# Kernel optimization log

Measured on AMD Instinct MI355X. Metric: run time of the kernel, lower is better.

Reference implementation:

```python
import jax, jax.numpy as jnp
import numpy as np

N = 50000   # nodes
E = 800000  # edges
G = 64      # graphs
D_IN = 128
D_OUT = 64
HID = 2 * D_OUT  # 128, hidden width of non-final layers
EPS = 1e-5


def _seg_sum(v, idx, n):
    return jax.ops.segment_sum(v, idx, num_segments=n)


def _gcn(x, W, b, src, dst, n):
    # GCNConv with default add_self_loops=True, edge_weight=1, sym norm
    xw = x @ W                                            # [N, out]
    deg = _seg_sum(jnp.ones(src.shape[0], x.dtype), dst, n) + 1.0  # +1 self loop
    dis = jax.lax.rsqrt(deg)                              # deg^{-1/2}, deg>=1
    norm = dis[src] * dis[dst]                            # [E]
    agg = _seg_sum(norm[:, None] * xw[src], dst, n)       # gather-scale-scatter
    return agg + (dis * dis)[:, None] * xw + b            # self-loop term + bias


def _mpnn_layer(x, src, dst, edge_attr, gw, gb, ew, eb, n):
    h = _gcn(x, gw, gb, src, dst, n)
    e = jax.nn.relu(edge_attr[:, None] * ew + eb)         # Linear(1,out).relu per edge
    msg = h[src] + e                                      # message = x_j + edge_attr
    cnt = _seg_sum(jnp.ones(src.shape[0], x.dtype), dst, n)
    return _seg_sum(msg, dst, n) / jnp.clip(cnt, 1.0)[:, None]  # scatter-mean


def _ln(x, g, b):
    # node-wise LayerNorm over feature dim
    mu = x.mean(-1, keepdims=True)
    var = x.var(-1, keepdims=True)
    return (x - mu) * jax.lax.rsqrt(var + EPS) * g + b


def setup_inputs() -> dict:
    key = jax.random.key(0)
    ks = jax.random.split(key, 24)
    x = jax.random.normal(ks[0], (N, D_IN), jnp.float32)
    edge_index = jax.random.randint(ks[1], (2, E), 0, N, dtype=jnp.int64)
    edge_attr = jax.random.uniform(ks[2], (E,), jnp.float32)
    batch = jnp.sort(jax.random.randint(ks[3], (N,), 0, G, dtype=jnp.int64))

    def lin(k, fan_in, shape):
        return jax.random.uniform(k, shape, jnp.float32, -1.0, 1.0) / np.sqrt(fan_in)

    # layer 0: in 128 -> 128; layer 1: 128 -> 128; layer 2: 128 -> 64
    inp = {
        "x": x, "edge_index": edge_index, "edge_attr": edge_attr, "batch": batch,
        "gcn_w0": lin(ks[4], D_IN, (D_IN, HID)),  "gcn_b0": jnp.zeros((HID,), jnp.float32),
        "edge_w0": lin(ks[5], 1, (HID,)),          "edge_b0": lin(ks[6], 1, (HID,)),
        "ln_g0": jnp.ones((HID,), jnp.float32),   "ln_b0": jnp.zeros((HID,), jnp.float32),
        "gcn_w1": lin(ks[7], HID, (HID, HID)),    "gcn_b1": jnp.zeros((HID,), jnp.float32),
        "edge_w1": lin(ks[8], 1, (HID,)),          "edge_b1": lin(ks[9], 1, (HID,)),
        "ln_g1": jnp.ones((HID,), jnp.float32),   "ln_b1": jnp.zeros((HID,), jnp.float32),
        "gcn_w2": lin(ks[10], HID, (HID, D_OUT)), "gcn_b2": jnp.zeros((D_OUT,), jnp.float32),
        "edge_w2": lin(ks[11], 1, (D_OUT,)),       "edge_b2": lin(ks[12], 1, (D_OUT,)),
    }
    return inp


def reference(x, edge_index, edge_attr, batch,
              gcn_w0, gcn_b0, edge_w0, edge_b0, ln_g0, ln_b0,
              gcn_w1, gcn_b1, edge_w1, edge_b1, ln_g1, ln_b1,
              gcn_w2, gcn_b2, edge_w2, edge_b2):
    src, dst = edge_index[0], edge_index[1]
    h = _mpnn_layer(x, src, dst, edge_attr, gcn_w0, gcn_b0, edge_w0, edge_b0, N)
    h = _ln(jax.nn.relu(h), ln_g0, ln_b0)
    h = _mpnn_layer(h, src, dst, edge_attr, gcn_w1, gcn_b1, edge_w1, edge_b1, N)
    h = _ln(jax.nn.relu(h), ln_g1, ln_b1)
    h = _mpnn_layer(h, src, dst, edge_attr, gcn_w2, gcn_b2, edge_w2, edge_b2, N)
    # global_mean_pool
    cnt = _seg_sum(jnp.ones((N,), h.dtype), batch, G)
    z_pooled = _seg_sum(h, batch, G) / jnp.clip(cnt, 1.0)[:, None]
    return h, z_pooled
```

## Files before the change

### kernel.cpp

```cpp
#include <hip/hip_runtime.h>

#define NN 50000
#define NE 800000
#define NG 64
#define HID 128
#define DOUT 64
#define LN_EPS 1e-5f
#define NBUK 391
#define BCAP 3072
#define EPB 2048

typedef unsigned int uint32;
typedef unsigned short ushort16;
typedef __attribute__((ext_vector_type(8))) short bf16x8;
typedef __attribute__((ext_vector_type(4))) float f32x4;

__device__ inline ushort16 f2bf(float f) {
  uint32 u = __float_as_uint(f);
  u += 0x7fffu + ((u >> 16) & 1u);
  return (ushort16)(u >> 16);
}
__device__ inline uint32 pack2(float x, float y) {
  return (uint32)f2bf(x) | ((uint32)f2bf(y) << 16);
}
__device__ inline float bflo(uint32 p) { return __uint_as_float(p << 16); }
__device__ inline float bfhi(uint32 p) { return __uint_as_float(p & 0xffff0000u); }

__global__ __launch_bounds__(256) void k_init(float* __restrict__ Z, int* __restrict__ bcur) {
  int i = blockIdx.x * 256 + threadIdx.x;
  if (i < NG * 64) Z[i] = 0.f;
  if (i < NBUK) bcur[i] = i * BCAP;
}

__global__ __launch_bounds__(1024) void k_bucket(const int* __restrict__ src,
                                                 const int* __restrict__ dst,
                                                 const float* __restrict__ ea,
                                                 int* __restrict__ bcur,
                                                 uint2* __restrict__ tmp, int e) {
  __shared__ int hist[NBUK], lbase[NBUK], lcur[NBUK];
  int t = threadIdx.x;
  for (int i = t; i < NBUK; i += 1024) {
    hist[i] = 0;
    lcur[i] = 0;
  }
  __syncthreads();
  int base_e = blockIdx.x * EPB;
  int dstv[EPB / 1024];
#pragma unroll
  for (int k = 0; k < EPB / 1024; k++) {
    int i = base_e + k * 1024 + t;
    int d = (i < e) ? dst[i] : -1;
    dstv[k] = d;
    if (d >= 0) atomicAdd(&hist[d >> 7], 1);
  }
  __syncthreads();
  for (int i = t; i < NBUK; i += 1024) {
    int c = hist[i];
    int b = 0;
    if (c > 0) b = atomicAdd(&bcur[i], c);
    lbase[i] = b;
  }
  __syncthreads();
#pragma unroll
  for (int k = 0; k < EPB / 1024; k++) {
    int i = base_e + k * 1024 + t;
    int d = dstv[k];
    if (d >= 0) {
      int b = d >> 7;
      int r = atomicAdd(&lcur[b], 1);
      int pos = lbase[b] + r;
      if (pos < (b + 1) * BCAP) {
        uint2 rec;
        rec.x = (uint32)(src[i] & 0xffff) | ((uint32)(d & 127) << 16);
        rec.y = __float_as_uint(ea[i]);
        tmp[pos] = rec;
      }
    }
  }
}

__global__ __launch_bounds__(512) void k_bscan(const int* __restrict__ bcur,
                                               int* __restrict__ bbase,
                                               int* __restrict__ rowptr) {
  __shared__ int s[512];
  int t = threadIdx.x;
  int v = 0;
  if (t < NBUK) {
    v = bcur[t] - t * BCAP;
    if (v > BCAP) v = BCAP;
  }
  s[t] = v;
  __syncthreads();
  for (int off = 1; off < 512; off <<= 1) {
    int x = (t >= off) ? s[t - off] : 0;
    __syncthreads();
    s[t] += x;
    __syncthreads();
  }
  if (t < NBUK) bbase[t] = s[t] - v;
  if (t == 511) {
    bbase[NBUK] = s[511];
    rowptr[NN] = s[511];
  }
}

__global__ __launch_bounds__(256) void k_bsort(const uint2* __restrict__ tmp,
                                               const int* __restrict__ bcur,
                                               const int* __restrict__ bbase,
                                               int* __restrict__ rowptr,
                                               int* __restrict__ csrc,
                                               uint2* __restrict__ emsg,
                                               float* __restrict__ dis,
                                               float* __restrict__ invc) {
  int b = blockIdx.x;
  __shared__ int hist[128], excl[128], cur[128];
  int t = threadIdx.x;
  if (t < 128) {
    hist[t] = 0;
    cur[t] = 0;
  }
  __syncthreads();
  int cnt = bcur[b] - b * BCAP;
  if (cnt > BCAP) cnt = BCAP;
  int tb = b * BCAP;
  int ob = bbase[b];
  for (int i = t; i < cnt; i += 256) {
    uint2 r = tmp[tb + i];
    atomicAdd(&hist[(r.x >> 16) & 127], 1);
  }
  __syncthreads();
  int myDeg = (t < 128) ? hist[t] : 0;
  for (int off = 1; off < 128; off <<= 1) {
    int x = 0;
    if (t < 128 && t >= off) x = hist[t - off];
    __syncthreads();
    if (t < 128) hist[t] += x;
    __syncthreads();
  }
  if (t < 128) {
    excl[t] = hist[t] - myDeg;
    int node = (b << 7) + t;
    if (node < NN) {
      rowptr[node] = ob + excl[t];
      dis[node] = rsqrtf((float)(myDeg + 1));
      invc[node] = (myDeg > 0) ? 1.0f / (float)myDeg : 1.0f;
    }
  }
  __syncthreads();
  for (int i = t; i < cnt; i += 256) {
    uint2 r = tmp[tb + i];
    int o = (r.x >> 16) & 127;
    int p = atomicAdd(&cur[o], 1);
    int pos = ob + excl[o] + p;
    int s = (int)(r.x & 0xffffu);
    csrc[pos] = s;
    emsg[pos] = make_uint2((uint32)s, r.y);
  }
}

template <int FOUT, bool IN_BF, bool OUT_BF>
__global__ __launch_bounds__(256) void k_gemm(const void* __restrict__ Xv,
                                              const float* __restrict__ W,
                                              const float* __restrict__ dis,
                                              void* __restrict__ Yv, int n) {
  const int NT = FOUT / 16;
  __shared__ __align__(16) unsigned short Wt[FOUT][136];
  __shared__ __align__(16) unsigned short Xs[64][136];
  int t = threadIdx.x;
  int row0 = blockIdx.x * 64;
  for (int idx = t; idx < 128 * FOUT; idx += 256) {
    int k = idx / FOUT, col = idx % FOUT;
    Wt[col][k] = (unsigned short)f2bf(W[idx]);
  }
  if (IN_BF) {
    const uint32* Xb = (const uint32*)Xv;
    for (int idx = t; idx < 64 * 64; idx += 256) {
      int r = idx >> 6, c = idx & 63;
      uint32 v = (row0 + r < n) ? Xb[(size_t)(row0 + r) * 64 + c] : 0u;
      *(uint32*)&Xs[r][c * 2] = v;
    }
  } else {
    const float* Xf = (const float*)Xv;
    for (int idx = t; idx < 64 * 64; idx += 256) {
      int r = idx >> 6, c = idx & 63;
      float2 v = make_float2(0.f, 0.f);
      if (row0 + r < n) v = ((const float2*)(Xf + (size_t)(row0 + r) * 128))[c];
      *(uint32*)&Xs[r][c * 2] = pack2(v.x, v.y);
    }
  }
  __syncthreads();
  int lane = t & 63, wv = t >> 6;
  int mrow = lane & 15, q = lane >> 4;
  f32x4 acc[NT];
#pragma unroll
  for (int c = 0; c < NT; c++) acc[c] = (f32x4){0.f, 0.f, 0.f, 0.f};
#pragma unroll
  for (int kt = 0; kt < 4; kt++) {
    bf16x8 af = *(const bf16x8*)&Xs[wv * 16 + mrow][kt * 32 + q * 8];
#pragma unroll
    for (int c = 0; c < NT; c++) {
      bf16x8 bfg = *(const bf16x8*)&Wt[c * 16 + mrow][kt * 32 + q * 8];
      acc[c] = __builtin_amdgcn_mfma_f32_16x16x32_bf16(af, bfg, acc[c], 0, 0, 0);
    }
  }
  float ds[4];
#pragma unroll
  for (int r = 0; r < 4; r++) {
    int rg = row0 + wv * 16 + q * 4 + r;
    ds[r] = (rg < n) ? dis[rg] : 0.f;
  }
#pragma unroll
  for (int c = 0; c < NT; c++) {
    int cg = c * 16 + mrow;
#pragma unroll
    for (int r = 0; r < 4; r++) {
      int rg = row0 + wv * 16 + q * 4 + r;
      if (rg < n) {
        float v = acc[c][r] * ds[r];
        if (OUT_BF)
          ((unsigned short*)Yv)[(size_t)rg * FOUT + cg] = (unsigned short)f2bf(v);
        else
          ((float*)Yv)[(size_t)rg * FOUT + cg] = v;
      }
    }
  }
}

__global__ __launch_bounds__(256) void k_agg_bf(const uint2* __restrict__ XW2,
                                                const float* __restrict__ dis,
                                                const int* __restrict__ rowptr,
                                                const int* __restrict__ csrc,
                                                const float* __restrict__ bias,
                                                uint2* __restrict__ Hb2, int n) {
  int l = threadIdx.x & 31;
  int node = blockIdx.x * 8 + (threadIdx.x >> 5);
  if (node >= n) return;
  float dn = dis[node];
  int beg = rowptr[node], end = rowptr[node + 1];
  float a0 = 0.f, a1 = 0.f, a2 = 0.f, a3 = 0.f;
  int i = beg;
  for (; i + 8 <= end; i += 8) {
    int s[8];
    uint2 p[8];
#pragma unroll
    for (int k = 0; k < 8; k++) s[k] = csrc[i + k];
#pragma unroll
    for (int k = 0; k < 8; k++) p[k] = XW2[(size_t)s[k] * 32 + l];
#pragma unroll
    for (int k = 0; k < 8; k++) {
      a0 += bflo(p[k].x);
      a1 += bfhi(p[k].x);
      a2 += bflo(p[k].y);
      a3 += bfhi(p[k].y);
    }
  }
  for (; i < end; i++) {
    uint2 p = XW2[(size_t)csrc[i] * 32 + l];
    a0 += bflo(p.x);
    a1 += bfhi(p.x);
    a2 += bflo(p.y);
    a3 += bfhi(p.y);
  }
  uint2 ps = XW2[(size_t)node * 32 + l];
  float4 bb = ((const float4*)bias)[l];
  float h0 = dn * (a0 + bflo(ps.x)) + bb.x;
  float h1 = dn * (a1 + bfhi(ps.x)) + bb.y;
  float h2 = dn * (a2 + bflo(ps.y)) + bb.z;
  float h3 = dn * (a3 + bfhi(ps.y)) + bb.w;
  Hb2[(size_t)node * 32 + l] = make_uint2(pack2(h0, h1), pack2(h2, h3));
}

__global__ __launch_bounds__(256) void k_msg_bf(const uint2* __restrict__ Hb2,
                                                const float* __restrict__ ew,
                                                const float* __restrict__ eb,
                                                const int* __restrict__ rowptr,
                                                const uint2* __restrict__ emsg,
                                                const float* __restrict__ invc,
                                                const float* __restrict__ lng,
                                                const float* __restrict__ lnb,
                                                uint2* __restrict__ OUTb2, int n) {
  int l = threadIdx.x & 31;
  int node = blockIdx.x * 8 + (threadIdx.x >> 5);
  if (node >= n) return;
  int beg = rowptr[node], end = rowptr[node + 1];
  float4 w = ((const float4*)ew)[l];
  float4 b = ((const float4*)eb)[l];
  float a0 = 0.f, a1 = 0.f, a2 = 0.f, a3 = 0.f;
  int i = beg;
  for (; i + 8 <= end; i += 8) {
    uint2 m[8];
    uint2 p[8];
#pragma unroll
    for (int k = 0; k < 8; k++) m[k] = emsg[i + k];
#pragma unroll
    for (int k = 0; k < 8; k++) p[k] = Hb2[(size_t)m[k].x * 32 + l];
#pragma unroll
    for (int k = 0; k < 8; k++) {
      float a = __uint_as_float(m[k].y);
      a0 += bflo(p[k].x) + fmaxf(a * w.x + b.x, 0.f);
      a1 += bfhi(p[k].x) + fmaxf(a * w.y + b.y, 0.f);
      a2 += bflo(p[k].y) + fmaxf(a * w.z + b.z, 0.f);
      a3 += bfhi(p[k].y) + fmaxf(a * w.w + b.w, 0.f);
    }
  }
  for (; i < end; i++) {
    uint2 m = emsg[i];
    uint2 p = Hb2[(size_t)m.x * 32 + l];
    float a = __uint_as_float(m.y);
    a0 += bflo(p.x) + fmaxf(a * w.x + b.x, 0.f);
    a1 += bfhi(p.x) + fmaxf(a * w.y + b.y, 0.f);
    a2 += bflo(p.y) + fmaxf(a * w.z + b.z, 0.f);
    a3 += bfhi(p.y) + fmaxf(a * w.w + b.w, 0.f);
  }
  float ic = invc[node];
  float o0 = fmaxf(a0 * ic, 0.f), o1 = fmaxf(a1 * ic, 0.f);
  float o2 = fmaxf(a2 * ic, 0.f), o3 = fmaxf(a3 * ic, 0.f);
  float s1 = o0 + o1 + o2 + o3;
  float s2 = o0 * o0 + o1 * o1 + o2 * o2 + o3 * o3;
#pragma unroll
  for (int off = 16; off; off >>= 1) {
    s1 += __shfl_xor(s1, off, 64);
    s2 += __shfl_xor(s2, off, 64);
  }
  float mu = s1 * (1.f / 128.f);
  float var = s2 * (1.f / 128.f) - mu * mu;
  float r = rsqrtf(var + LN_EPS);
  float4 g = ((const float4*)lng)[l];
  float4 bb = ((const float4*)lnb)[l];
  o0 = (o0 - mu) * r * g.x + bb.x;
  o1 = (o1 - mu) * r * g.y + bb.y;
  o2 = (o2 - mu) * r * g.z + bb.z;
  o3 = (o3 - mu) * r * g.w + bb.w;
  OUTb2[(size_t)node * 32 + l] = make_uint2(pack2(o0, o1), pack2(o2, o3));
}

__global__ __launch_bounds__(256) void k_agg64b(const uint32* __restrict__ XWb,
                                                const float* __restrict__ dis,
                                                const int* __restrict__ rowptr,
                                                const int* __restrict__ csrc,
                                                const float* __restrict__ bias,
                                                uint32* __restrict__ Hb, int n) {
  int l = threadIdx.x & 31;
  int node = blockIdx.x * 8 + (threadIdx.x >> 5);
  if (node >= n) return;
  float dn = dis[node];
  int beg = rowptr[node], end = rowptr[node + 1];
  float a0 = 0.f, a1 = 0.f;
  int i = beg;
  for (; i + 8 <= end; i += 8) {
    int s[8];
    uint32 p[8];
#pragma unroll
    for (int k = 0; k < 8; k++) s[k] = csrc[i + k];
#pragma unroll
    for (int k = 0; k < 8; k++) p[k] = XWb[(size_t)s[k] * 32 + l];
#pragma unroll
    for (int k = 0; k < 8; k++) {
      a0 += bflo(p[k]);
      a1 += bfhi(p[k]);
    }
  }
  for (; i < end; i++) {
    uint32 p = XWb[(size_t)csrc[i] * 32 + l];
    a0 += bflo(p);
    a1 += bfhi(p);
  }
  uint32 ps = XWb[(size_t)node * 32 + l];
  float2 bb = ((const float2*)bias)[l];
  float h0 = dn * (a0 + bflo(ps)) + bb.x;
  float h1 = dn * (a1 + bfhi(ps)) + bb.y;
  Hb[(size_t)node * 32 + l] = pack2(h0, h1);
}

__global__ __launch_bounds__(256) void k_msg64b(const uint32* __restrict__ Hb,
                                                const float* __restrict__ ew,
                                                const float* __restrict__ eb,
                                                const int* __restrict__ rowptr,
                                                const uint2* __restrict__ emsg,
                                                const float* __restrict__ invc,
                                                float* __restrict__ OUT, int n) {
  int l = threadIdx.x & 31;
  int node = blockIdx.x * 8 + (threadIdx.x >> 5);
  if (node >= n) return;
  int beg = rowptr[node], end = rowptr[node + 1];
  float2 w = ((const float2*)ew)[l];
  float2 b = ((const float2*)eb)[l];
  float a0 = 0.f, a1 = 0.f;
  int i = beg;
  for (; i + 8 <= end; i += 8) {
    uint2 m[8];
    uint32 p[8];
#pragma unroll
    for (int k = 0; k < 8; k++) m[k] = emsg[i + k];
#pragma unroll
    for (int k = 0; k < 8; k++) p[k] = Hb[(size_t)m[k].x * 32 + l];
#pragma unroll
    for (int k = 0; k < 8; k++) {
      float a = __uint_as_float(m[k].y);
      a0 += bflo(p[k]) + fmaxf(a * w.x + b.x, 0.f);
      a1 += bfhi(p[k]) + fmaxf(a * w.y + b.y, 0.f);
    }
  }
  for (; i < end; i++) {
    uint2 m = emsg[i];
    uint32 p = Hb[(size_t)m.x * 32 + l];
    float a = __uint_as_float(m.y);
    a0 += bflo(p) + fmaxf(a * w.x + b.x, 0.f);
    a1 += bfhi(p) + fmaxf(a * w.y + b.y, 0.f);
  }
  float ic = invc[node];
  ((float2*)OUT)[(size_t)node * 32 + l] = make_float2(a0 * ic, a1 * ic);
}

#define POOL_BLOCKS 256
__global__ __launch_bounds__(256) void k_pool_partial(const float* __restrict__ H,
                                                      const int* __restrict__ batch,
                                                      float* __restrict__ Z, int n) {
  int lane = threadIdx.x & 63;
  int wid = blockIdx.x * 4 + (threadIdx.x >> 6);
  const int WAVES = POOL_BLOCKS * 4;
  int per = (n + WAVES - 1) / WAVES;
  int beg = wid * per;
  int end = beg + per;
  if (end > n) end = n;
  if (beg >= end) return;
  int g = batch[beg];
  float acc = 0.f;
  for (int i = beg; i < end; i++) {
    int gi = batch[i];
    if (gi != g) {
      atomicAdd(&Z[g * 64 + lane], acc);
      acc = 0.f;
      g = gi;
    }
    acc += H[(size_t)i * 64 + lane];
  }
  atomicAdd(&Z[g * 64 + lane], acc);
}

__global__ __launch_bounds__(64) void k_pool_div(float* __restrict__ Z,
                                                 const int* __restrict__ batch, int n) {
  int g = blockIdx.x;
  __shared__ int scnt;
  if (threadIdx.x == 0) {
    int lo = 0, hi = n;
    while (lo < hi) { int m = (lo + hi) >> 1; if (batch[m] < g) lo = m + 1; else hi = m; }
    int b0 = lo;
    lo = 0; hi = n;
    while (lo < hi) { int m = (lo + hi) >> 1; if (batch[m] < g + 1) lo = m + 1; else hi = m; }
    scnt = lo - b0;
  }
  __syncthreads();
  float c = (float)scnt;
  if (c < 1.f) c = 1.f;
  Z[g * 64 + threadIdx.x] /= c;
}

extern "C" void kernel_launch(void* const* d_in, const int* in_sizes, int n_in,
                              void* d_out, int out_size, void* d_ws, size_t ws_size,
                              hipStream_t stream) {
  const float* x = (const float*)d_in[0];
  const int* ei = (const int*)d_in[1];
  const float* ea = (const float*)d_in[2];
  const int* batch = (const int*)d_in[3];
  const float* gw0 = (const float*)d_in[4];
  const float* gb0 = (const float*)d_in[5];
  const float* ew0 = (const float*)d_in[6];
  const float* eb0 = (const float*)d_in[7];
  const float* lg0 = (const float*)d_in[8];
  const float* lb0 = (const float*)d_in[9];
  const float* gw1 = (const float*)d_in[10];
  const float* gb1 = (const float*)d_in[11];
  const float* ew1 = (const float*)d_in[12];
  const float* eb1 = (const float*)d_in[13];
  const float* lg1 = (const float*)d_in[14];
  const float* lb1 = (const float*)d_in[15];
  const float* gw2 = (const float*)d_in[16];
  const float* gb2 = (const float*)d_in[17];
  const float* ew2 = (const float*)d_in[18];
  const float* eb2 = (const float*)d_in[19];
  float* out = (float*)d_out;

  const int* src = ei;
  const int* dst = ei + NE;

  char* w = (char*)d_ws;
  size_t off = 0;
  auto alloc = [&](size_t bytes) -> void* {
    void* p = (void*)(w + off);
    off = (off + bytes + 255) & ~(size_t)255;
    return p;
  };
  int* rowptr = (int*)alloc((NN + 1) * sizeof(int));
  int* bcur = (int*)alloc(NBUK * sizeof(int));
  int* bbase = (int*)alloc((NBUK + 1) * sizeof(int));
  int* csrc = (int*)alloc(NE * sizeof(int));
  uint2* emsg = (uint2*)alloc(NE * sizeof(uint2));
  float* dis = (float*)alloc(NN * sizeof(float));
  float* invc = (float*)alloc(NN * sizeof(float));
  uint2* B1b = (uint2*)alloc((size_t)NN * 32 * sizeof(uint2));
  uint2* B2b = (uint2*)alloc((size_t)NN * 32 * sizeof(uint2));
  uint32* F1b = (uint32*)alloc((size_t)NN * 32 * sizeof(uint32));
  uint32* F2b = (uint32*)alloc((size_t)NN * 32 * sizeof(uint32));
  uint2* tmp = (uint2*)alloc((size_t)NBUK * BCAP * sizeof(uint2));

  float* Z = out + (size_t)NN * 64;

  hipLaunchKernelGGL(k_init, dim3((NG * 64 + 255) / 256), dim3(256), 0, stream, Z, bcur);
  hipLaunchKernelGGL(k_bucket, dim3((NE + EPB - 1) / EPB), dim3(1024), 0, stream, src, dst, ea,
                     bcur, tmp, NE);
  hipLaunchKernelGGL(k_bscan, dim3(1), dim3(512), 0, stream, bcur, bbase, rowptr);
  hipLaunchKernelGGL(k_bsort, dim3(NBUK), dim3(256), 0, stream, tmp, bcur, bbase, rowptr, csrc,
                     emsg, dis, invc);

  dim3 gemm_grid((NN + 63) / 64), tb(256);
  dim3 node_grid((NN + 7) / 8);

  hipLaunchKernelGGL((k_gemm<128, false, true>), gemm_grid, tb, 0, stream, x, gw0, dis, B1b, NN);
  hipLaunchKernelGGL(k_agg_bf, node_grid, tb, 0, stream, B1b, dis, rowptr, csrc, gb0, B2b, NN);
  hipLaunchKernelGGL(k_msg_bf, node_grid, tb, 0, stream, B2b, ew0, eb0, rowptr, emsg, invc,
                     lg0, lb0, B1b, NN);
  hipLaunchKernelGGL((k_gemm<128, true, true>), gemm_grid, tb, 0, stream, B1b, gw1, dis, B2b, NN);
  hipLaunchKernelGGL(k_agg_bf, node_grid, tb, 0, stream, B2b, dis, rowptr, csrc, gb1, B1b, NN);
  hipLaunchKernelGGL(k_msg_bf, node_grid, tb, 0, stream, B1b, ew1, eb1, rowptr, emsg, invc,
                     lg1, lb1, B2b, NN);
  hipLaunchKernelGGL((k_gemm<64, true, true>), gemm_grid, tb, 0, stream, B2b, gw2, dis, F1b, NN);
  hipLaunchKernelGGL(k_agg64b, node_grid, tb, 0, stream, F1b, dis, rowptr, csrc, gb2, F2b, NN);
  hipLaunchKernelGGL(k_msg64b, node_grid, tb, 0, stream, F2b, ew2, eb2, rowptr, emsg, invc,
                     out, NN);
  hipLaunchKernelGGL(k_pool_partial, dim3(POOL_BLOCKS), tb, 0, stream, out, batch, Z, NN);
  hipLaunchKernelGGL(k_pool_div, dim3(NG), dim3(64), 0, stream, Z, batch, NN);
}
```

Measured before the change: 427.1 us.

## Split gather kernels into feature-column slices and defer LayerNorm into next GEMM

The aggregation and message kernels now process each node in two feature halves, with consecutive blocks (slice = blockIdx.x & 1) covering the two halves of the same nodes. Each block's gathers therefore touch a narrower column band of the feature table, which is meant to improve cache locality and give more parallel blocks. Because LayerNorm needs full-row statistics, the message kernel now writes partial sums, a new small kernel combines them into mean and inverse std, and the normalisation is applied while loading inputs in the following GEMM. The cost is extra launches, duplicated index and edge-record reads across slices, and extra traffic for the statistics buffers.

Result: slower. 487.7 us (+14.2%).

```diff
diff --git a/kernel.cpp b/kernel.cpp
--- a/kernel.cpp
+++ b/kernel.cpp
@@ -158,11 +158,14 @@
   }
 }
 
-template <int FOUT, bool IN_BF, bool OUT_BF>
+template <int FOUT, bool IN_BF, bool LN_IN>
 __global__ __launch_bounds__(256) void k_gemm(const void* __restrict__ Xv,
                                               const float* __restrict__ W,
                                               const float* __restrict__ dis,
-                                              void* __restrict__ Yv, int n) {
+                                              const float2* __restrict__ musd,
+                                              const float* __restrict__ lng,
+                                              const float* __restrict__ lnb,
+                                              unsigned short* __restrict__ Yv, int n) {
   const int NT = FOUT / 16;
   __shared__ __align__(16) unsigned short Wt[FOUT][136];
   __shared__ __align__(16) unsigned short Xs[64][136];
@@ -176,8 +179,22 @@
     const uint32* Xb = (const uint32*)Xv;
     for (int idx = t; idx < 64 * 64; idx += 256) {
       int r = idx >> 6, c = idx & 63;
-      uint32 v = (row0 + r < n) ? Xb[(size_t)(row0 + r) * 64 + c] : 0u;
-      *(uint32*)&Xs[r][c * 2] = v;
+      int rg = row0 + r;
+      uint32 v = 0u;
+      float2 ms = make_float2(0.f, 0.f);
+      if (rg < n) {
+        v = Xb[(size_t)rg * 64 + c];
+        if (LN_IN) ms = musd[rg];
+      }
+      if (LN_IN) {
+        float2 g = ((const float2*)lng)[c];
+        float2 q = ((const float2*)lnb)[c];
+        float lo = (bflo(v) - ms.x) * ms.y * g.x + q.x;
+        float hi = (bfhi(v) - ms.x) * ms.y * g.y + q.y;
+        *(uint32*)&Xs[r][c * 2] = pack2(lo, hi);
+      } else {
+        *(uint32*)&Xs[r][c * 2] = v;
+      }
     }
   } else {
     const float* Xf = (const float*)Xv;
@@ -215,134 +232,22 @@
 #pragma unroll
     for (int r = 0; r < 4; r++) {
       int rg = row0 + wv * 16 + q * 4 + r;
-      if (rg < n) {
-        float v = acc[c][r] * ds[r];
-        if (OUT_BF)
-          ((unsigned short*)Yv)[(size_t)rg * FOUT + cg] = (unsigned short)f2bf(v);
-        else
-          ((float*)Yv)[(size_t)rg * FOUT + cg] = v;
-      }
-    }
-  }
-}
-
-__global__ __launch_bounds__(256) void k_agg_bf(const uint2* __restrict__ XW2,
+      if (rg < n) Yv[(size_t)rg * FOUT + cg] = (unsigned short)f2bf(acc[c][r] * ds[r]);
+    }
+  }
+}
+
+__global__ __launch_bounds__(256) void k_agg_bf(const uint32* __restrict__ XW,
                                                 const float* __restrict__ dis,
                                                 const int* __restrict__ rowptr,
                                                 const int* __restrict__ csrc,
                                                 const float* __restrict__ bias,
-                                                uint2* __restrict__ Hb2, int n) {
+                                                uint32* __restrict__ H, int n) {
+  int slice = blockIdx.x & 1;
   int l = threadIdx.x & 31;
-  int node = blockIdx.x * 8 + (threadIdx.x >> 5);
+  int node = (blockIdx.x >> 1) * 8 + (threadIdx.x >> 5);
   if (node >= n) return;
-  float dn = dis[node];
-  int beg = rowptr[node], end = rowptr[node + 1];
-  float a0 = 0.f, a1 = 0.f, a2 = 0.f, a3 = 0.f;
-  int i = beg;
-  for (; i + 8 <= end; i += 8) {
-    int s[8];
-    uint2 p[8];
-#pragma unroll
-    for (int k = 0; k < 8; k++) s[k] = csrc[i + k];
-#pragma unroll
-    for (int k = 0; k < 8; k++) p[k] = XW2[(size_t)s[k] * 32 + l];
-#pragma unroll
-    for (int k = 0; k < 8; k++) {
-      a0 += bflo(p[k].x);
-      a1 += bfhi(p[k].x);
-      a2 += bflo(p[k].y);
-      a3 += bfhi(p[k].y);
-    }
-  }
-  for (; i < end; i++) {
-    uint2 p = XW2[(size_t)csrc[i] * 32 + l];
-    a0 += bflo(p.x);
-    a1 += bfhi(p.x);
-    a2 += bflo(p.y);
-    a3 += bfhi(p.y);
-  }
-  uint2 ps = XW2[(size_t)node * 32 + l];
-  float4 bb = ((const float4*)bias)[l];
-  float h0 = dn * (a0 + bflo(ps.x)) + bb.x;
-  float h1 = dn * (a1 + bfhi(ps.x)) + bb.y;
-  float h2 = dn * (a2 + bflo(ps.y)) + bb.z;
-  float h3 = dn * (a3 + bfhi(ps.y)) + bb.w;
-  Hb2[(size_t)node * 32 + l] = make_uint2(pack2(h0, h1), pack2(h2, h3));
-}
-
-__global__ __launch_bounds__(256) void k_msg_bf(const uint2* __restrict__ Hb2,
-                                                const float* __restrict__ ew,
-                                                const float* __restrict__ eb,
-                                                const int* __restrict__ rowptr,
-                                                const uint2* __restrict__ emsg,
-                                                const float* __restrict__ invc,
-                                                const float* __restrict__ lng,
-                                                const float* __restrict__ lnb,
-                                                uint2* __restrict__ OUTb2, int n) {
-  int l = threadIdx.x & 31;
-  int node = blockIdx.x * 8 + (threadIdx.x >> 5);
-  if (node >= n) return;
-  int beg = rowptr[node], end = rowptr[node + 1];
-  float4 w = ((const float4*)ew)[l];
-  float4 b = ((const float4*)eb)[l];
-  float a0 = 0.f, a1 = 0.f, a2 = 0.f, a3 = 0.f;
-  int i = beg;
-  for (; i + 8 <= end; i += 8) {
-    uint2 m[8];
-    uint2 p[8];
-#pragma unroll
-    for (int k = 0; k < 8; k++) m[k] = emsg[i + k];
-#pragma unroll
-    for (int k = 0; k < 8; k++) p[k] = Hb2[(size_t)m[k].x * 32 + l];
-#pragma unroll
-    for (int k = 0; k < 8; k++) {
-      float a = __uint_as_float(m[k].y);
-      a0 += bflo(p[k].x) + fmaxf(a * w.x + b.x, 0.f);
-      a1 += bfhi(p[k].x) + fmaxf(a * w.y + b.y, 0.f);
-      a2 += bflo(p[k].y) + fmaxf(a * w.z + b.z, 0.f);
-      a3 += bfhi(p[k].y) + fmaxf(a * w.w + b.w, 0.f);
-    }
-  }
-  for (; i < end; i++) {
-    uint2 m = emsg[i];
-    uint2 p = Hb2[(size_t)m.x * 32 + l];
-    float a = __uint_as_float(m.y);
-    a0 += bflo(p.x) + fmaxf(a * w.x + b.x, 0.f);
-    a1 += bfhi(p.x) + fmaxf(a * w.y + b.y, 0.f);
-    a2 += bflo(p.y) + fmaxf(a * w.z + b.z, 0.f);
-    a3 += bfhi(p.y) + fmaxf(a * w.w + b.w, 0.f);
-  }
-  float ic = invc[node];
-  float o0 = fmaxf(a0 * ic, 0.f), o1 = fmaxf(a1 * ic, 0.f);
-  float o2 = fmaxf(a2 * ic, 0.f), o3 = fmaxf(a3 * ic, 0.f);
-  float s1 = o0 + o1 + o2 + o3;
-  float s2 = o0 * o0 + o1 * o1 + o2 * o2 + o3 * o3;
-#pragma unroll
-  for (int off = 16; off; off >>= 1) {
-    s1 += __shfl_xor(s1, off, 64);
-    s2 += __shfl_xor(s2, off, 64);
-  }
-  float mu = s1 * (1.f / 128.f);
-  float var = s2 * (1.f / 128.f) - mu * mu;
-  float r = rsqrtf(var + LN_EPS);
-  float4 g = ((const float4*)lng)[l];
-  float4 bb = ((const float4*)lnb)[l];
-  o0 = (o0 - mu) * r * g.x + bb.x;
-  o1 = (o1 - mu) * r * g.y + bb.y;
-  o2 = (o2 - mu) * r * g.z + bb.z;
-  o3 = (o3 - mu) * r * g.w + bb.w;
-  OUTb2[(size_t)node * 32 + l] = make_uint2(pack2(o0, o1), pack2(o2, o3));
-}
-
-__global__ __launch_bounds__(256) void k_agg64b(const uint32* __restrict__ XWb,
-                                                const float* __restrict__ dis,
-                                                const int* __restrict__ rowptr,
-                                                const int* __restrict__ csrc,
-                                                const float* __restrict__ bias,
-                                                uint32* __restrict__ Hb, int n) {
-  int l = threadIdx.x & 31;
-  int node = blockIdx.x * 8 + (threadIdx.x >> 5);
-  if (node >= n) return;
+  const uint32* T = XW + slice * 32 + l;
   float dn = dis[node];
   int beg = rowptr[node], end = rowptr[node + 1];
   float a0 = 0.f, a1 = 0.f;
@@ -353,7 +258,7 @@
 #pragma unroll
     for (int k = 0; k < 8; k++) s[k] = csrc[i + k];
 #pragma unroll
-    for (int k = 0; k < 8; k++) p[k] = XWb[(size_t)s[k] * 32 + l];
+    for (int k = 0; k < 8; k++) p[k] = T[(size_t)s[k] * 64];
 #pragma unroll
     for (int k = 0; k < 8; k++) {
       a0 += bflo(p[k]);
@@ -361,15 +266,119 @@
     }
   }
   for (; i < end; i++) {
-    uint32 p = XWb[(size_t)csrc[i] * 32 + l];
+    uint32 p = T[(size_t)csrc[i] * 64];
     a0 += bflo(p);
     a1 += bfhi(p);
   }
-  uint32 ps = XWb[(size_t)node * 32 + l];
-  float2 bb = ((const float2*)bias)[l];
+  uint32 ps = T[(size_t)node * 64];
+  float2 bb = ((const float2*)bias)[slice * 32 + l];
   float h0 = dn * (a0 + bflo(ps)) + bb.x;
   float h1 = dn * (a1 + bfhi(ps)) + bb.y;
-  Hb[(size_t)node * 32 + l] = pack2(h0, h1);
+  H[(size_t)node * 64 + slice * 32 + l] = pack2(h0, h1);
+}
+
+__global__ __launch_bounds__(256) void k_msg_bf(const uint32* __restrict__ Hb,
+                                                const float* __restrict__ ew,
+                                                const float* __restrict__ eb,
+                                                const int* __restrict__ rowptr,
+                                                const uint2* __restrict__ emsg,
+                                                const float* __restrict__ invc,
+                                                uint32* __restrict__ OUT,
+                                                float2* __restrict__ s1s2, int n) {
+  int slice = blockIdx.x & 1;
+  int l = threadIdx.x & 31;
+  int node = (blockIdx.x >> 1) * 8 + (threadIdx.x >> 5);
+  if (node >= n) return;
+  const uint32* T = Hb + slice * 32 + l;
+  int beg = rowptr[node], end = rowptr[node + 1];
+  float2 w = ((const float2*)ew)[slice * 32 + l];
+  float2 b = ((const float2*)eb)[slice * 32 + l];
+  float a0 = 0.f, a1 = 0.f;
+  int i = beg;
+  for (; i + 8 <= end; i += 8) {
+    uint2 m[8];
+    uint32 p[8];
+#pragma unroll
+    for (int k = 0; k < 8; k++) m[k] = emsg[i + k];
+#pragma unroll
+    for (int k = 0; k < 8; k++) p[k] = T[(size_t)m[k].x * 64];
+#pragma unroll
+    for (int k = 0; k < 8; k++) {
+      float e = __uint_as_float(m[k].y);
+      a0 += bflo(p[k]) + fmaxf(e * w.x + b.x, 0.f);
+      a1 += bfhi(p[k]) + fmaxf(e * w.y + b.y, 0.f);
+    }
+  }
+  for (; i < end; i++) {
+    uint2 m = emsg[i];
+    uint32 p = T[(size_t)m.x * 64];
+    float e = __uint_as_float(m.y);
+    a0 += bflo(p) + fmaxf(e * w.x + b.x, 0.f);
+    a1 += bfhi(p) + fmaxf(e * w.y + b.y, 0.f);
+  }
+  float ic = invc[node];
+  float o0 = fmaxf(a0 * ic, 0.f);
+  float o1 = fmaxf(a1 * ic, 0.f);
+  OUT[(size_t)node * 64 + slice * 32 + l] = pack2(o0, o1);
+  float s1 = o0 + o1, s2 = o0 * o0 + o1 * o1;
+#pragma unroll
+  for (int off = 16; off; off >>= 1) {
+    s1 += __shfl_xor(s1, off, 64);
+    s2 += __shfl_xor(s2, off, 64);
+  }
+  if (l == 0) s1s2[(size_t)node * 2 + slice] = make_float2(s1, s2);
+}
+
+__global__ __launch_bounds__(256) void k_lnstat(const float2* __restrict__ s1s2,
+                                                float2* __restrict__ musd, int n) {
+  int i = blockIdx.x * 256 + threadIdx.x;
+  if (i < n) {
+    float2 a = s1s2[(size_t)i * 2];
+    float2 b = s1s2[(size_t)i * 2 + 1];
+    float mu = (a.x + b.x) * (1.f / 128.f);
+    float var = (a.y + b.y) * (1.f / 128.f) - mu * mu;
+    musd[i] = make_float2(mu, rsqrtf(var + LN_EPS));
+  }
+}
+
+__global__ __launch_bounds__(256) void k_agg64b(const uint32* __restrict__ XW,
+                                                const float* __restrict__ dis,
+                                                const int* __restrict__ rowptr,
+                                                const int* __restrict__ csrc,
+                                                const float* __restrict__ bias,
+                                                uint32* __restrict__ H, int n) {
+  int slice = blockIdx.x & 1;
+  int l = threadIdx.x & 15;
+  int node = (blockIdx.x >> 1) * 16 + (threadIdx.x >> 4);
+  if (node >= n) return;
+  const uint32* T = XW + slice * 16 + l;
+  float dn = dis[node];
+  int beg = rowptr[node], end = rowptr[node + 1];
+  float a0 = 0.f, a1 = 0.f;
+  int i = beg;
+  for (; i + 8 <= end; i += 8) {
+    int s[8];
+    uint32 p[8];
+#pragma unroll
+    for (int k = 0; k < 8; k++) s[k] = csrc[i + k];
+#pragma unroll
+    for (int k = 0; k < 8; k++) p[k] = T[(size_t)s[k] * 32];
+#pragma unroll
+    for (int k = 0; k < 8; k++) {
+      a0 += bflo(p[k]);
+      a1 += bfhi(p[k]);
+    }
+  }
+  for (; i < end; i++) {
+    uint32 p = T[(size_t)csrc[i] * 32];
+    a0 += bflo(p);
+    a1 += bfhi(p);
+  }
+  uint32 ps = T[(size_t)node * 32];
+  float2 bb = ((const float2*)bias)[slice * 16 + l];
+  float h0 = dn * (a0 + bflo(ps)) + bb.x;
+  float h1 = dn * (a1 + bfhi(ps)) + bb.y;
+  H[(size_t)node * 32 + slice * 16 + l] = pack2(h0, h1);
 }
 
 __global__ __launch_bounds__(256) void k_msg64b(const uint32* __restrict__ Hb,
@@ -379,12 +388,14 @@
                                                 const uint2* __restrict__ emsg,
                                                 const float* __restrict__ invc,
                                                 float* __restrict__ OUT, int n) {
-  int l = threadIdx.x & 31;
-  int node = blockIdx.x * 8 + (threadIdx.x >> 5);
+  int slice = blockIdx.x & 1;
+  int l = threadIdx.x & 15;
+  int node = (blockIdx.x >> 1) * 16 + (threadIdx.x >> 4);
   if (node >= n) return;
+  const uint32* T = Hb + slice * 16 + l;
   int beg = rowptr[node], end = rowptr[node + 1];
-  float2 w = ((const float2*)ew)[l];
-  float2 b = ((const float2*)eb)[l];
+  float2 w = ((const float2*)ew)[slice * 16 + l];
+  float2 b = ((const float2*)eb)[slice * 16 + l];
   float a0 = 0.f, a1 = 0.f;
   int i = beg;
   for (; i + 8 <= end; i += 8) {
@@ -393,23 +404,23 @@
 #pragma unroll
     for (int k = 0; k < 8; k++) m[k] = emsg[i + k];
 #pragma unroll
-    for (int k = 0; k < 8; k++) p[k] = Hb[(size_t)m[k].x * 32 + l];
+    for (int k = 0; k < 8; k++) p[k] = T[(size_t)m[k].x * 32];
 #pragma unroll
     for (int k = 0; k < 8; k++) {
-      float a = __uint_as_float(m[k].y);
-      a0 += bflo(p[k]) + fmaxf(a * w.x + b.x, 0.f);
-      a1 += bfhi(p[k]) + fmaxf(a * w.y + b.y, 0.f);
+      float e = __uint_as_float(m[k].y);
+      a0 += bflo(p[k]) + fmaxf(e * w.x + b.x, 0.f);
+      a1 += bfhi(p[k]) + fmaxf(e * w.y + b.y, 0.f);
     }
   }
   for (; i < end; i++) {
     uint2 m = emsg[i];
-    uint32 p = Hb[(size_t)m.x * 32 + l];
-    float a = __uint_as_float(m.y);
-    a0 += bflo(p) + fmaxf(a * w.x + b.x, 0.f);
-    a1 += bfhi(p) + fmaxf(a * w.y + b.y, 0.f);
+    uint32 p = T[(size_t)m.x * 32];
+    float e = __uint_as_float(m.y);
+    a0 += bflo(p) + fmaxf(e * w.x + b.x, 0.f);
+    a1 += bfhi(p) + fmaxf(e * w.y + b.y, 0.f);
   }
   float ic = invc[node];
-  ((float2*)OUT)[(size_t)node * 32 + l] = make_float2(a0 * ic, a1 * ic);
+  ((float2*)OUT)[(size_t)node * 32 + slice * 16 + l] = make_float2(a0 * ic, a1 * ic);
 }
 
 #define POOL_BLOCKS 256
@@ -498,8 +509,10 @@
   uint2* emsg = (uint2*)alloc(NE * sizeof(uint2));
   float* dis = (float*)alloc(NN * sizeof(float));
   float* invc = (float*)alloc(NN * sizeof(float));
-  uint2* B1b = (uint2*)alloc((size_t)NN * 32 * sizeof(uint2));
-  uint2* B2b = (uint2*)alloc((size_t)NN * 32 * sizeof(uint2));
+  float2* s1s2 = (float2*)alloc((size_t)NN * 2 * sizeof(float2));
+  float2* musd = (float2*)alloc((size_t)NN * sizeof(float2));
+  uint32* B1b = (uint32*)alloc((size_t)NN * 64 * sizeof(uint32));
+  uint32* B2b = (uint32*)alloc((size_t)NN * 64 * sizeof(uint32));
   uint32* F1b = (uint32*)alloc((size_t)NN * 32 * sizeof(uint32));
   uint32* F2b = (uint32*)alloc((size_t)NN * 32 * sizeof(uint32));
   uint2* tmp = (uint2*)alloc((size_t)NBUK * BCAP * sizeof(uint2));
@@ -514,20 +527,26 @@
                      emsg, dis, invc);
 
   dim3 gemm_grid((NN + 63) / 64), tb(256);
-  dim3 node_grid((NN + 7) / 8);
-
-  hipLaunchKernelGGL((k_gemm<128, false, true>), gemm_grid, tb, 0, stream, x, gw0, dis, B1b, NN);
-  hipLaunchKernelGGL(k_agg_bf, node_grid, tb, 0, stream, B1b, dis, rowptr, csrc, gb0, B2b, NN);
-  hipLaunchKernelGGL(k_msg_bf, node_grid, tb, 0, stream, B2b, ew0, eb0, rowptr, emsg, invc,
-                     lg0, lb0, B1b, NN);
-  hipLaunchKernelGGL((k_gemm<128, true, true>), gemm_grid, tb, 0, stream, B1b, gw1, dis, B2b, NN);
-  hipLaunchKernelGGL(k_agg_bf, node_grid, tb, 0, stream, B2b, dis, rowptr, csrc, gb1, B1b, NN);
-  hipLaunchKernelGGL(k_msg_bf, node_grid, tb, 0, stream, B1b, ew1, eb1, rowptr, emsg, invc,
-                     lg1, lb1, B2b, NN);
-  hipLaunchKernelGGL((k_gemm<64, true, true>), gemm_grid, tb, 0, stream, B2b, gw2, dis, F1b, NN);
-  hipLaunchKernelGGL(k_agg64b, node_grid, tb, 0, stream, F1b, dis, rowptr, csrc, gb2, F2b, NN);
-  hipLaunchKernelGGL(k_msg64b, node_grid, tb, 0, stream, F2b, ew2, eb2, rowptr, emsg, invc,
-                     out, NN);
+  dim3 g128(2 * ((NN + 7) / 8));
+  dim3 g64(2 * ((NN + 15) / 16));
+  dim3 gstat((NN + 255) / 256);
+
+  hipLaunchKernelGGL((k_gemm<128, false, false>), gemm_grid, tb, 0, stream, x, gw0, dis,
+                     nullptr, nullptr, nullptr, (unsigned short*)B1b, NN);
+  hipLaunchKernelGGL(k_agg_bf, g128, tb, 0, stream, B1b, dis, rowptr, csrc, gb0, B2b, NN);
+  hipLaunchKernelGGL(k_msg_bf, g128, tb, 0, stream, B2b, ew0, eb0, rowptr, emsg, invc, B1b,
+                     s1s2, NN);
+  hipLaunchKernelGGL(k_lnstat, gstat, tb, 0, stream, s1s2, musd, NN);
+  hipLaunchKernelGGL((k_gemm<128, true, true>), gemm_grid, tb, 0, stream, B1b, gw1, dis, musd,
+                     lg0, lb0, (unsigned short*)B2b, NN);
+  hipLaunchKernelGGL(k_agg_bf, g128, tb, 0, stream, B2b, dis, rowptr, csrc, gb1, B1b, NN);
+  hipLaunchKernelGGL(k_msg_bf, g128, tb, 0, stream, B1b, ew1, eb1, rowptr, emsg, invc, B2b,
+                     s1s2, NN);
+  hipLaunchKernelGGL(k_lnstat, gstat, tb, 0, stream, s1s2, musd, NN);
+  hipLaunchKernelGGL((k_gemm<64, true, true>), gemm_grid, tb, 0, stream, B2b, gw2, dis, musd,
+                     lg1, lb1, (unsigned short*)F1b, NN);
+  hipLaunchKernelGGL(k_agg64b, g64, tb, 0, stream, F1b, dis, rowptr, csrc, gb2, F2b, NN);
+  hipLaunchKernelGGL(k_msg64b, g64, tb, 0, stream, F2b, ew2, eb2, rowptr, emsg, invc, out, NN);
   hipLaunchKernelGGL(k_pool_partial, dim3(POOL_BLOCKS), tb, 0, stream, out, batch, Z, NN);
   hipLaunchKernelGGL(k_pool_div, dim3(NG), dim3(64), 0, stream, Z, batch, NN);
 }
```
